# Optimization experiments

Measured on AMD Instinct MI355X. Metric: run time of the kernel, lower is better.

Reference implementation:

```python
import jax, jax.numpy as jnp
import numpy as np

N_WIRES = 9
N_QRAM_LAYERS = 3
N_QCLS_LAYERS = 5

X = jnp.array([[0, 1], [1, 0]], dtype=jnp.complex64)
CNOT = jnp.array([[1, 0, 0, 0], [0, 1, 0, 0], [0, 0, 0, 1], [0, 0, 1, 0]], dtype=jnp.complex64)


def _rx(t):
    c = jnp.cos(t / 2)
    s = jnp.sin(t / 2)
    # works for scalar t -> (2,2) or batched t [B] -> (B,2,2)
    return jnp.stack([jnp.stack([c + 0j, -1j * s], -1), jnp.stack([-1j * s, c + 0j], -1)], -2)


def _ry(t):
    c = jnp.cos(t / 2)
    s = jnp.sin(t / 2)
    return jnp.stack([jnp.stack([c, -s], -1), jnp.stack([s, c], -1)], -2).astype(jnp.complex64)


def _rz(t):
    e = jnp.exp(-0.5j * t)
    f = jnp.exp(0.5j * t)
    z = jnp.zeros_like(e)
    return jnp.stack([jnp.stack([e, z], -1), jnp.stack([z, f], -1)], -2)


def _rot(phi, theta, omega):
    # PennyLane Rot(phi, theta, omega) = RZ(omega) @ RY(theta) @ RZ(phi)
    return _rz(omega) @ _ry(theta) @ _rz(phi)


def _crz(t):
    e = jnp.exp(-0.5j * t)
    f = jnp.exp(0.5j * t)
    one = jnp.ones((), e.dtype)
    return jnp.diag(jnp.stack([one, one, e, f]))


def _crx(t):
    return jnp.eye(4, dtype=jnp.complex64).at[2:, 2:].set(_rx(t))


def apply_1q(state, U, w):
    # state: [B] + (2,)*N_WIRES ; wire w -> axis 1+w
    s = jnp.moveaxis(state, 1 + w, -1)
    if U.ndim == 3:  # per-sample gate (embedding)
        s = jnp.einsum('bij,b...j->b...i', U, s)
    else:
        s = jnp.einsum('ij,...j->...i', U, s)
    return jnp.moveaxis(s, -1, 1 + w)


def apply_2q(state, U, c, t):
    s = jnp.moveaxis(state, (1 + c, 1 + t), (-2, -1))
    shp = s.shape
    s = s.reshape(shp[:-2] + (4,))
    s = jnp.einsum('ij,...j->...i', U, s)
    return jnp.moveaxis(s.reshape(shp), (-2, -1), (1 + c, 1 + t))


def embed(state, adds):
    # AngleEmbedding: RX(adds[:, i]) on wire i
    for i in range(N_WIRES):
        state = apply_1q(state, _rx(adds[:, i]), i)
    return state


def entangle_block(state, p):
    # p: [36] = 4 params per wire-pair step
    j = 0
    for i in range(N_WIRES):
        ip = (i + 1) % N_WIRES
        state = apply_1q(state, _ry(p[j]), i)
        state = apply_1q(state, _ry(p[j + 1]), ip)
        state = apply_2q(state, CNOT, i, ip)
        state = apply_2q(state, _crz(p[j + 2]), i, ip)
        state = apply_1q(state, X, ip)
        state = apply_2q(state, _crx(p[j + 3]), i, ip)
        j += 4
    return state


def sel_layer(state, w, r):
    # one StronglyEntanglingLayers layer: Rot on each wire, then CNOT ring of range r
    for i in range(N_WIRES):
        state = apply_1q(state, _rot(w[i, 0], w[i, 1], w[i, 2]), i)
    for i in range(N_WIRES):
        state = apply_2q(state, CNOT, i, (i + r) % N_WIRES)
    return state


def circuit(adds, params, weights, params2):
    B = adds.shape[0]
    state = jnp.zeros((B,) + (2,) * N_WIRES, jnp.complex64)
    state = state.at[(slice(None),) + (0,) * N_WIRES].set(1.0)
    state = embed(state, adds)
    for l in range(N_QRAM_LAYERS):
        state = entangle_block(state, params[l * 36:(l + 1) * 36])
    for l in range(N_QRAM_LAYERS):
        r = (l % (N_WIRES - 1)) + 1  # PennyLane default ranges
        state = sel_layer(state, weights[l], r)
    for l in range(N_QCLS_LAYERS):
        state = entangle_block(state, params2[l * 36:(l + 1) * 36])
    probs = jnp.abs(state) ** 2
    p = probs.reshape(B, 2, -1).sum(-1)  # marginal over wire 0
    return p[:, 0] - p[:, 1]  # <PauliZ(0)>


def setup_inputs() -> dict:
    key = jax.random.key(0)
    k1, k2, k3, k4 = jax.random.split(key, 4)
    B = 8192
    return {
        'adds': jax.random.normal(k1, (B, N_WIRES), dtype=jnp.float32),
        'params': jax.random.normal(k2, (N_QRAM_LAYERS * 36,), dtype=jnp.float32),
        'weights': jax.random.normal(k3, (N_QRAM_LAYERS, N_WIRES, N_QRAM_LAYERS), dtype=jnp.float32),
        'params2': jax.random.normal(k4, (N_QCLS_LAYERS * 36,), dtype=jnp.float32),
    }


def reference(adds, params, weights, params2):
    return circuit(adds, params, weights, params2)
```

## Files before the change

### kernel.cpp

```cpp
#include <hip/hip_runtime.h>

#define NQ 9
#define NS 512
#define M2 1024

#define COEF_ROT_BASE (72*32)
#define COEF_R3_BASE  (COEF_ROT_BASE + 27*8)
#define COEF_FLOATS   (COEF_R3_BASE + 3*128)

typedef __attribute__((ext_vector_type(8))) short bf16x8;
typedef __attribute__((ext_vector_type(4))) float f32x4;

__device__ inline unsigned short f2bf(float f){
  unsigned int u = __float_as_uint(f);
  u += 0x7fffu + ((u >> 16) & 1u);
  return (unsigned short)(u >> 16);
}


template<int LM>
__device__ inline float lxor(float v){
  if constexpr (LM == 1)
    return __int_as_float(__builtin_amdgcn_mov_dpp(__float_as_int(v), 0xB1, 0xF, 0xF, true));
  else if constexpr (LM == 2)
    return __int_as_float(__builtin_amdgcn_mov_dpp(__float_as_int(v), 0x4E, 0xF, 0xF, true));
  else if constexpr (LM == 3)
    return __int_as_float(__builtin_amdgcn_mov_dpp(__float_as_int(v), 0x1B, 0xF, 0xF, true));
  else if constexpr (LM < 32)
    return __int_as_float(__builtin_amdgcn_ds_swizzle(__float_as_int(v), (LM<<10)|0x1F));
  else
    return __shfl_xor(v, LM);
}

template<int CM, int TM>
__device__ inline void step_h(float& ax, float& ay, int i, float2* buf,
                              const float* g){
  buf[i] = make_float2(ax, ay);
  __syncthreads();
  float2 tv = buf[i ^ TM];
  float2 cv = buf[i ^ CM];
  float2 bv = buf[i ^ (CM ^ TM)];
  int p = ((i & CM) ? 2 : 0) | ((i & TM) ? 1 : 0);
  float4 hx = *(const float4*)(g + p*4);
  float4 hy = *(const float4*)(g + 16 + p*4);
  float ox = ax, oy = ay;
  ax = hx.x*ox - hy.x*oy + hx.y*tv.x - hy.y*tv.y
     + hx.z*cv.x - hy.z*cv.y + hx.w*bv.x - hy.w*bv.y;
  ay = hx.x*oy + hy.x*ox + hx.y*tv.y + hy.y*tv.x
     + hx.z*cv.y + hy.z*cv.x + hx.w*bv.y + hy.w*bv.x;
}

template<int CM, int TM>
__device__ inline void step_swz(float& ax, float& ay, int lane, const float* g){
  float tx = lxor<TM>(ax),      ty = lxor<TM>(ay);
  float cx = lxor<CM>(ax),      cy = lxor<CM>(ay);
  float bx = lxor<(CM^TM)>(ax), by = lxor<(CM^TM)>(ay);
  int p = ((lane & CM) ? 2 : 0) | ((lane & TM) ? 1 : 0);
  float4 hx = *(const float4*)(g + p*4);
  float4 hy = *(const float4*)(g + 16 + p*4);
  float ox = ax, oy = ay;
  ax = hx.x*ox - hy.x*oy + hx.y*tx - hy.y*ty
     + hx.z*cx - hy.z*cy + hx.w*bx - hy.w*by;
  ay = hx.x*oy + hy.x*ox + hx.y*ty + hy.y*tx
     + hx.z*cy + hy.z*cx + hx.w*by + hy.w*bx;
}

__device__ inline void rot3_img(float& ax, float& ay, int i, float2* buf,
                                const float* M){
  buf[i] = make_float2(ax, ay);
  __syncthreads();
  int base = i & 63;
  float nx = 0.f, ny = 0.f;
  #pragma unroll
  for (int q = 0; q < 8; ++q){
    float2 v = buf[(q << 6) | base];
    float mx = M[q*2], my = M[q*2+1];
    nx += mx*v.x - my*v.y;
    ny += mx*v.y + my*v.x;
  }
  ax = nx; ay = ny;
}

template<int LM>
__device__ inline void rot_swz(float& ax, float& ay, int lane, const float* u){
  float px = lxor<LM>(ax), py = lxor<LM>(ay);
  float4 uu = *(const float4*)(u + ((lane & LM) ? 4 : 0));
  float nx = uu.x*ax - uu.y*ay + uu.z*px - uu.w*py;
  float ny = uu.x*ay + uu.y*ax + uu.z*py + uu.w*px;
  ax = nx; ay = ny;
}

__device__ inline void ring_rt(float& ax, float& ay, int i, float2* buf, int R){
  buf[i] = make_float2(ax, ay);
  __syncthreads();
  int s = i;
  for (int k = 8; k >= 0; --k){
    int bc = 8 - k;
    int it = k + R; if (it >= 9) it -= 9;
    int bt = 8 - it;
    s ^= ((s >> bc) & 1) << bt;
  }
  float2 v = buf[s];
  ax = v.x; ay = v.y;
}


template<int I = 0>
__device__ inline void ent_blk(float& ax, float& ay, int i, int lane,
                               float2* bufA, float2* bufB, const float* S){
  const float* g = S + I*32;
  if constexpr      (I == 0) step_h<0x100,0x080>(ax, ay, i, bufA, g);
  else if constexpr (I == 1) step_h<0x080,0x040>(ax, ay, i, bufB, g);
  else if constexpr (I == 2) step_h<0x040,0x020>(ax, ay, i, bufA, g);
  else if constexpr (I == 8) step_h<0x001,0x100>(ax, ay, i, bufB, g);
  else                       step_swz<(1<<(8-I)),(1<<(7-I))>(ax, ay, lane, g);
  if constexpr (I < 8) ent_blk<I+1>(ax, ay, i, lane, bufA, bufB, S);
}

template<int I = 3>
__device__ inline void sel_lane_rots(float& ax, float& ay, int lane,
                                     const float* ub){
  rot_swz<(1<<(8-I))>(ax, ay, lane, ub + I*8);
  if constexpr (I < 8) sel_lane_rots<I+1>(ax, ay, lane, ub);
}

__global__ __launch_bounds__(512) void sim_prep(const float* __restrict__ params,
                                                const float* __restrict__ weights,
                                                const float* __restrict__ params2,
                                                const float* __restrict__ adds,
                                                unsigned short* __restrict__ A2,
                                                unsigned short* __restrict__ cT,
                                                float* __restrict__ out, int B){
  int tid = threadIdx.x;

  if (blockIdx.x >= NS){
    int gid = (blockIdx.x - NS) * 512 + tid;
    int b = gid >> 6;
    int lane = gid & 63;
    if (b < B){
      const float* ab = adds + b * NQ;
      float cw[NQ], sw[NQ];
      #pragma unroll
      for (int w = 0; w < NQ; ++w)
        __sincosf(0.5f * ab[w], &sw[w], &cw[w]);
      float p6 = 1.f;
      #pragma unroll
      for (int w = 0; w < 6; ++w)
        p6 *= ((lane >> (5 - w)) & 1) ? sw[w] : cw[w];
      union { unsigned short u[8]; uint4 v; } pk;
      #pragma unroll
      for (int j = 0; j < 8; ++j){
        float p = p6 * (((j>>2)&1) ? sw[6] : cw[6])
                     * (((j>>1)&1) ? sw[7] : cw[7])
                     * (( j    &1) ? sw[8] : cw[8]);
        pk.u[j] = f2bf(p);
      }
      *(uint4*)(cT + (size_t)b * NS + lane*8) = pk.v;
    }
    if (gid < B) out[gid] = 0.f;
    return;
  }

  __shared__ float2 bufA[512];
  __shared__ float2 bufB[512];
  __shared__ float scoef[COEF_FLOATS];

  if (tid < 72){
    int blk = tid / 9, I = tid % 9;
    const float* p = (blk < 3) ? params + blk*36 : params2 + (blk-3)*36;
    float s0,c0,s1,c1,s2,c2,s3,c3;
    __sincosf(0.5f*p[4*I+0], &s0, &c0);
    __sincosf(0.5f*p[4*I+1], &s1, &c1);
    __sincosf(0.5f*p[4*I+2], &s2, &c2);
    __sincosf(0.5f*p[4*I+3], &s3, &c3);
    float m[4][4] = {
      { c0*c1, -c0*s1, -s0*c1,  s0*s1},
      { c0*s1,  c0*c1, -s0*s1, -s0*c1},
      { s0*c1, -s0*s1,  c0*c1, -c0*s1},
      { s0*s1,  s0*c1,  c0*s1,  c0*c1}};
    float gx[4][4], gy[4][4];
    #pragma unroll
    for (int q = 0; q < 4; ++q){
      gx[0][q] = m[1][q];  gy[0][q] = 0.f;
      gx[1][q] = m[0][q];  gy[1][q] = 0.f;
      gx[2][q] =  c3*c2*m[2][q] - s3*s2*m[3][q];
      gy[2][q] =  c3*s2*m[2][q] - s3*c2*m[3][q];
      gx[3][q] =  s3*s2*m[2][q] + c3*c2*m[3][q];
      gy[3][q] = -(s3*c2*m[2][q] + c3*s2*m[3][q]);
    }
    float* dst = scoef + tid*32;
    #pragma unroll
    for (int pp = 0; pp < 4; ++pp)
      #pragma unroll
      for (int d = 0; d < 4; ++d){
        dst[pp*4+d]    = gx[pp][pp^d];
        dst[16+pp*4+d] = gy[pp][pp^d];
      }
  } else if (tid < 99){
    int r = tid - 72;
    int l = r / 9, i = r % 9;
    const float* w = weights + l*27 + 3*i;
    float phi = w[0], th = w[1], om = w[2];
    float sT,cT,sA,cA,sB,cB;
    __sincosf(0.5f*th, &sT, &cT);
    __sincosf(0.5f*(phi+om), &sA, &cA);
    __sincosf(0.5f*(om-phi), &sB, &cB);
    float* dst = scoef + COEF_ROT_BASE + r*8;
    dst[0] =  cA*cT;  dst[1] = -sA*cT;
    dst[2] = -cB*sT;  dst[3] =  sB*sT;
    dst[4] =  cA*cT;  dst[5] =  sA*cT;
    dst[6] =  cB*sT;  dst[7] =  sB*sT;
  } else if (tid < 123){
    int idx = tid - 99;
    int l = idx >> 3, p = idx & 7;
    float e0x[3], e0y[3], e1x[3], e1y[3];
    #pragma unroll
    for (int w = 0; w < 3; ++w){
      const float* wp = weights + l*27 + 3*w;
      float phi = wp[0], th = wp[1], om = wp[2];
      float sT,cT,sA,cA,sB,cB;
      __sincosf(0.5f*th, &sT, &cT);
      __sincosf(0.5f*(phi+om), &sA, &cA);
      __sincosf(0.5f*(om-phi), &sB, &cB);
      int pw = (p >> (2 - w)) & 1;
      if (pw == 0){ e0x[w] =  cA*cT; e0y[w] = -sA*cT; e1x[w] = -cB*sT; e1y[w] =  sB*sT; }
      else        { e0x[w] =  cB*sT; e0y[w] =  sB*sT; e1x[w] =  cA*cT; e1y[w] =  sA*cT; }
    }
    float* dst = scoef + COEF_R3_BASE + l*128 + p*16;
    #pragma unroll
    for (int q = 0; q < 8; ++q){
      float rx = 1.f, ry = 0.f;
      #pragma unroll
      for (int w = 0; w < 3; ++w){
        int qw = (q >> (2 - w)) & 1;
        float fx = qw ? e1x[w] : e0x[w];
        float fy = qw ? e1y[w] : e0y[w];
        float nx = rx*fx - ry*fy;
        float ny = rx*fy + ry*fx;
        rx = nx; ry = ny;
      }
      dst[q*2]   = rx;
      dst[q*2+1] = ry;
    }
  }
  __syncthreads();

  int t = blockIdx.x;
  int i = tid;
  int lane = tid & 63;
  float ax, ay;
  int pc = __popc((unsigned)t) & 3;
  float prx = (pc==0) ? 1.f : (pc==2 ? -1.f : 0.f);
  float pry = (pc==3) ? 1.f : (pc==1 ? -1.f : 0.f);
  ax = (i == t) ? prx : 0.f;
  ay = (i == t) ? pry : 0.f;

  #pragma unroll 1
  for (int blk = 0; blk < 3; ++blk)
    ent_blk<0>(ax, ay, i, lane, bufA, bufB, scoef + blk*288);
  #pragma unroll 1
  for (int L = 0; L < 3; ++L){
    rot3_img(ax, ay, i, bufA, scoef + COEF_R3_BASE + L*128 + (i>>6)*16);
    sel_lane_rots<3>(ax, ay, lane, scoef + COEF_ROT_BASE + L*72);
    ring_rt(ax, ay, i, bufB, L + 1);
  }
  #pragma unroll 1
  for (int blk = 3; blk < 8; ++blk)
    ent_blk<0>(ax, ay, i, lane, bufA, bufB, scoef + blk*288);

  A2[(size_t)i * NS + t]        = f2bf(ax);
  A2[(size_t)(i + NS) * NS + t] = f2bf(ay);
}

__global__ __launch_bounds__(256) void gemm_out(const unsigned short* __restrict__ A2,
                                                const unsigned short* __restrict__ cT,
                                                float* __restrict__ out){
  int bx = blockIdx.x;
  int by = blockIdx.y;
  int tid = threadIdx.x;
  int wave = tid >> 6, lane = tid & 63;
  int wy = wave >> 1, wx = wave & 1;
  int lane15 = lane & 15, quad = lane >> 4;
  int rowBase = by*128 + wy*64;
  int colBase = bx*128 + wx*64;
  const short* Ap = (const short*)A2;
  const short* Bp = (const short*)cT;

  f32x4 acc[4][4];
  #pragma unroll
  for (int i = 0; i < 4; ++i)
    #pragma unroll
    for (int j = 0; j < 4; ++j)
      acc[i][j] = (f32x4){0.f, 0.f, 0.f, 0.f};

  #pragma unroll 2
  for (int k0 = 0; k0 < NS; k0 += 32){
    bf16x8 a[4], b[4];
    #pragma unroll
    for (int mi = 0; mi < 4; ++mi)
      a[mi] = *(const bf16x8*)(Ap + (size_t)(rowBase + mi*16 + lane15)*NS + k0 + quad*8);
    #pragma unroll
    for (int ni = 0; ni < 4; ++ni)
      b[ni] = *(const bf16x8*)(Bp + (size_t)(colBase + ni*16 + lane15)*NS + k0 + quad*8);
    #pragma unroll
    for (int mi = 0; mi < 4; ++mi)
      #pragma unroll
      for (int ni = 0; ni < 4; ++ni)
        acc[mi][ni] = __builtin_amdgcn_mfma_f32_16x16x32_bf16(a[mi], b[ni], acc[mi][ni], 0, 0, 0);
  }

  float sign = (by & 2) ? -1.f : 1.f;
  #pragma unroll
  for (int ni = 0; ni < 4; ++ni){
    float cs = 0.f;
    #pragma unroll
    for (int mi = 0; mi < 4; ++mi)
      #pragma unroll
      for (int r = 0; r < 4; ++r)
        cs += acc[mi][ni][r] * acc[mi][ni][r];
    cs += __shfl_xor(cs, 16);
    cs += __shfl_xor(cs, 32);
    if (quad == 0)
      atomicAdd(out + colBase + ni*16 + lane15, sign * cs);
  }
}

extern "C" void kernel_launch(void* const* d_in, const int* in_sizes, int n_in,
                              void* d_out, int out_size, void* d_ws, size_t ws_size,
                              hipStream_t stream) {
  const float* adds    = (const float*)d_in[0];
  const float* params  = (const float*)d_in[1];
  const float* weights = (const float*)d_in[2];
  const float* params2 = (const float*)d_in[3];
  float* out = (float*)d_out;
  int B = in_sizes[0] / NQ;

  unsigned short* A2 = (unsigned short*)d_ws;
  unsigned short* cT = A2 + (size_t)M2 * NS;

  int prepBlocks = (B * 64 + 511) / 512;
  hipLaunchKernelGGL(sim_prep, dim3(NS + prepBlocks), dim3(512), 0, stream,
                     params, weights, params2, adds, A2, cT, out, B);
  hipLaunchKernelGGL(gemm_out, dim3(B / 128, 8), dim3(256), 0, stream, A2, cT, out);
}
```

Measured before the change: 118.2 us.

## Merge cross-wave entangler steps into dense 16x16 and 8x8 shared-memory matrices

Each entangler block previously did four separate shared-memory exchange steps, each with a barrier. The three leading two-qubit steps (wires 0-3) are now premultiplied into one 16x16 complex matrix, and the last two steps (wires 7,8,0) into one 8x8 matrix. Each block then needs two barriered shared-memory passes instead of four, at the cost of more FLOPs per element and extra setup to build the matrices. The A2 matrix is also stored in a k-chunked layout so the GEMM loads contiguous bf16x8 vectors, and the GEMM unroll is raised.

```diff
diff --git a/kernel.cpp b/kernel.cpp
--- a/kernel.cpp
+++ b/kernel.cpp
@@ -3,10 +3,14 @@
 #define NQ 9
 #define NS 512
 #define M2 1024
-
-#define COEF_ROT_BASE (72*32)
-#define COEF_R3_BASE  (COEF_ROT_BASE + 27*8)
-#define COEF_FLOATS   (COEF_R3_BASE + 3*128)
+#define NSIMB 512
+
+#define ENT_H_BASE 0
+#define ROT_BASE   1024
+#define ROT3_BASE  1240
+#define M0123_BASE 1624
+#define M78_BASE   5720
+#define COEF_FLOATS 6744
 
 typedef __attribute__((ext_vector_type(8))) short bf16x8;
 typedef __attribute__((ext_vector_type(4))) float f32x4;
@@ -30,24 +34,6 @@
     return __int_as_float(__builtin_amdgcn_ds_swizzle(__float_as_int(v), (LM<<10)|0x1F));
   else
     return __shfl_xor(v, LM);
-}
-
-template<int CM, int TM>
-__device__ inline void step_h(float& ax, float& ay, int i, float2* buf,
-                              const float* g){
-  buf[i] = make_float2(ax, ay);
-  __syncthreads();
-  float2 tv = buf[i ^ TM];
-  float2 cv = buf[i ^ CM];
-  float2 bv = buf[i ^ (CM ^ TM)];
-  int p = ((i & CM) ? 2 : 0) | ((i & TM) ? 1 : 0);
-  float4 hx = *(const float4*)(g + p*4);
-  float4 hy = *(const float4*)(g + 16 + p*4);
-  float ox = ax, oy = ay;
-  ax = hx.x*ox - hy.x*oy + hx.y*tv.x - hy.y*tv.y
-     + hx.z*cv.x - hy.z*cv.y + hx.w*bv.x - hy.w*bv.y;
-  ay = hx.x*oy + hy.x*ox + hx.y*tv.y + hy.y*tv.x
-     + hx.z*cv.y + hy.z*cv.x + hx.w*bv.y + hy.w*bv.x;
 }
 
 template<int CM, int TM>
@@ -65,20 +51,62 @@
      + hx.z*cy + hy.z*cx + hx.w*by + hy.w*bx;
 }
 
-__device__ inline void rot3_img(float& ax, float& ay, int i, float2* buf,
-                                const float* M){
-  buf[i] = make_float2(ax, ay);
-  __syncthreads();
+__device__ inline void mrg16(float& ax, float& ay, int i, float2* xb, const float* Mt){
+  xb[i] = make_float2(ax, ay);
+  __syncthreads();
+  int p = (i >> 5) & 15;
+  const float* Mr = Mt + p*32;
+  int base = i & 31;
+  float s0x=0.f,s0y=0.f,s1x=0.f,s1y=0.f;
+  #pragma unroll
+  for (int q = 0; q < 16; q += 2){
+    float2 v0 = xb[(q<<5)|base];
+    float2 v1 = xb[((q+1)<<5)|base];
+    float m0x = Mr[q*2],   m0y = Mr[q*2+1];
+    float m1x = Mr[q*2+2], m1y = Mr[q*2+3];
+    s0x += m0x*v0.x - m0y*v0.y;  s0y += m0x*v0.y + m0y*v0.x;
+    s1x += m1x*v1.x - m1y*v1.y;  s1y += m1x*v1.y + m1y*v1.x;
+  }
+  ax = s0x + s1x; ay = s0y + s1y;
+}
+
+__device__ inline void mrg8_78(float& ax, float& ay, int i, float2* xb, const float* Mt){
+  xb[i] = make_float2(ax, ay);
+  __syncthreads();
+  int p = (((i>>1)&1)<<2) | ((i&1)<<1) | ((i>>8)&1);
+  const float* Mr = Mt + p*16;
+  int ib = i & 0x0FC;
+  float s0x=0.f,s0y=0.f,s1x=0.f,s1y=0.f;
+  #pragma unroll
+  for (int q = 0; q < 8; q += 2){
+    int j0 = ib | ((q>>2)<<1) | ((q>>1)&1);
+    float2 v0 = xb[j0];
+    float2 v1 = xb[j0 | 0x100];
+    float m0x = Mr[q*2],   m0y = Mr[q*2+1];
+    float m1x = Mr[q*2+2], m1y = Mr[q*2+3];
+    s0x += m0x*v0.x - m0y*v0.y;  s0y += m0x*v0.y + m0y*v0.x;
+    s1x += m1x*v1.x - m1y*v1.y;  s1y += m1x*v1.y + m1y*v1.x;
+  }
+  ax = s0x + s1x; ay = s0y + s1y;
+}
+
+__device__ inline void rot3R(float& ax, float& ay, int i, float2* xb, const float* Mt){
+  xb[i] = make_float2(ax, ay);
+  __syncthreads();
+  int p = i >> 6;
+  const float* Mr = Mt + p*16;
   int base = i & 63;
-  float nx = 0.f, ny = 0.f;
+  float s0x=0.f,s0y=0.f,s1x=0.f,s1y=0.f;
   #pragma unroll
-  for (int q = 0; q < 8; ++q){
-    float2 v = buf[(q << 6) | base];
-    float mx = M[q*2], my = M[q*2+1];
-    nx += mx*v.x - my*v.y;
-    ny += mx*v.y + my*v.x;
-  }
-  ax = nx; ay = ny;
+  for (int q = 0; q < 8; q += 2){
+    float2 v0 = xb[(q<<6)|base];
+    float2 v1 = xb[((q+1)<<6)|base];
+    float m0x = Mr[q*2],   m0y = Mr[q*2+1];
+    float m1x = Mr[q*2+2], m1y = Mr[q*2+3];
+    s0x += m0x*v0.x - m0y*v0.y;  s0y += m0x*v0.y + m0y*v0.x;
+    s1x += m1x*v1.x - m1y*v1.y;  s1y += m1x*v1.y + m1y*v1.x;
+  }
+  ax = s0x + s1x; ay = s0y + s1y;
 }
 
 template<int LM>
@@ -90,6 +118,12 @@
   ax = nx; ay = ny;
 }
 
+template<int I = 3>
+__device__ inline void sel_lane_rots(float& ax, float& ay, int lane, const float* ub){
+  rot_swz<(1<<(8-I))>(ax, ay, lane, ub + I*8);
+  if constexpr (I < 8) sel_lane_rots<I+1>(ax, ay, lane, ub);
+}
+
 __device__ inline void ring_rt(float& ax, float& ay, int i, float2* buf, int R){
   buf[i] = make_float2(ax, ay);
   __syncthreads();
@@ -104,25 +138,16 @@
   ax = v.x; ay = v.y;
 }
 
-
-template<int I = 0>
-__device__ inline void ent_blk(float& ax, float& ay, int i, int lane,
-                               float2* bufA, float2* bufB, const float* S){
-  const float* g = S + I*32;
-  if constexpr      (I == 0) step_h<0x100,0x080>(ax, ay, i, bufA, g);
-  else if constexpr (I == 1) step_h<0x080,0x040>(ax, ay, i, bufB, g);
-  else if constexpr (I == 2) step_h<0x040,0x020>(ax, ay, i, bufA, g);
-  else if constexpr (I == 8) step_h<0x001,0x100>(ax, ay, i, bufB, g);
-  else                       step_swz<(1<<(8-I)),(1<<(7-I))>(ax, ay, lane, g);
-  if constexpr (I < 8) ent_blk<I+1>(ax, ay, i, lane, bufA, bufB, S);
-}
-
-template<int I = 3>
-__device__ inline void sel_lane_rots(float& ax, float& ay, int lane,
-                                     const float* ub){
-  rot_swz<(1<<(8-I))>(ax, ay, lane, ub + I*8);
-  if constexpr (I < 8) sel_lane_rots<I+1>(ax, ay, lane, ub);
-}
+__device__ inline void entM(float& ax, float& ay, int i, int lane,
+                            float2* bA, float2* bB, const float* scoef, int blk){
+  mrg16(ax, ay, i, bA, scoef + M0123_BASE + blk*512);
+  step_swz<32,16>(ax, ay, lane, scoef + ENT_H_BASE + (blk*4+0)*32);
+  step_swz<16, 8>(ax, ay, lane, scoef + ENT_H_BASE + (blk*4+1)*32);
+  step_swz< 8, 4>(ax, ay, lane, scoef + ENT_H_BASE + (blk*4+2)*32);
+  step_swz< 4, 2>(ax, ay, lane, scoef + ENT_H_BASE + (blk*4+3)*32);
+  mrg8_78(ax, ay, i, bB, scoef + M78_BASE + blk*128);
+}
+
 
 __global__ __launch_bounds__(512) void sim_prep(const float* __restrict__ params,
                                                 const float* __restrict__ weights,
@@ -133,8 +158,8 @@
                                                 float* __restrict__ out, int B){
   int tid = threadIdx.x;
 
-  if (blockIdx.x >= NS){
-    int gid = (blockIdx.x - NS) * 512 + tid;
+  if (blockIdx.x >= NSIMB){
+    int gid = (blockIdx.x - NSIMB) * 512 + tid;
     int b = gid >> 6;
     int lane = gid & 63;
     if (b < B){
@@ -161,9 +186,11 @@
     return;
   }
 
-  __shared__ float2 bufA[512];
-  __shared__ float2 bufB[512];
+  __shared__ float2 ebuf[1024];
   __shared__ float scoef[COEF_FLOATS];
+  float2* ebufA = ebuf;
+  float2* ebufB = ebuf + 512;
+  float* graw = (float*)ebuf;
 
   if (tid < 72){
     int blk = tid / 9, I = tid % 9;
@@ -188,14 +215,26 @@
       gx[3][q] =  s3*s2*m[2][q] + c3*c2*m[3][q];
       gy[3][q] = -(s3*c2*m[2][q] + c3*s2*m[3][q]);
     }
-    float* dst = scoef + tid*32;
-    #pragma unroll
-    for (int pp = 0; pp < 4; ++pp)
-      #pragma unroll
-      for (int d = 0; d < 4; ++d){
-        dst[pp*4+d]    = gx[pp][pp^d];
-        dst[16+pp*4+d] = gy[pp][pp^d];
-      }
+    if (I >= 3 && I <= 6){
+      float* dst = scoef + ENT_H_BASE + (blk*4 + (I-3))*32;
+      #pragma unroll
+      for (int pp = 0; pp < 4; ++pp)
+        #pragma unroll
+        for (int d = 0; d < 4; ++d){
+          dst[pp*4+d]    = gx[pp][pp^d];
+          dst[16+pp*4+d] = gy[pp][pp^d];
+        }
+    } else {
+      float* dst = (I < 3) ? graw + (blk*3 + I)*32
+                           : graw + 768 + (blk*2 + (I-7))*32;
+      #pragma unroll
+      for (int pp = 0; pp < 4; ++pp)
+        #pragma unroll
+        for (int q = 0; q < 4; ++q){
+          dst[(pp*4+q)*2]   = gx[pp][q];
+          dst[(pp*4+q)*2+1] = gy[pp][q];
+        }
+    }
   } else if (tid < 99){
     int r = tid - 72;
     int l = r / 9, i = r % 9;
@@ -205,7 +244,7 @@
     __sincosf(0.5f*th, &sT, &cT);
     __sincosf(0.5f*(phi+om), &sA, &cA);
     __sincosf(0.5f*(om-phi), &sB, &cB);
-    float* dst = scoef + COEF_ROT_BASE + r*8;
+    float* dst = scoef + ROT_BASE + r*8;
     dst[0] =  cA*cT;  dst[1] = -sA*cT;
     dst[2] = -cB*sT;  dst[3] =  sB*sT;
     dst[4] =  cA*cT;  dst[5] =  sA*cT;
@@ -226,7 +265,7 @@
       if (pw == 0){ e0x[w] =  cA*cT; e0y[w] = -sA*cT; e1x[w] = -cB*sT; e1y[w] =  sB*sT; }
       else        { e0x[w] =  cB*sT; e0y[w] =  sB*sT; e1x[w] =  cA*cT; e1y[w] =  sA*cT; }
     }
-    float* dst = scoef + COEF_R3_BASE + l*128 + p*16;
+    float* dst = scoef + ROT3_BASE + l*128 + p*16;
     #pragma unroll
     for (int q = 0; q < 8; ++q){
       float rx = 1.f, ry = 0.f;
@@ -245,31 +284,80 @@
   }
   __syncthreads();
 
-  int t = blockIdx.x;
-  int i = tid;
-  int lane = tid & 63;
+  {
+    int blk = tid >> 6;
+    const float* G0 = graw + (blk*3+0)*32;
+    const float* G1 = graw + (blk*3+1)*32;
+    const float* G2 = graw + (blk*3+2)*32;
+    int e4 = (tid & 63) * 4;
+    #pragma unroll
+    for (int k = 0; k < 4; ++k){
+      int e = e4 + k;
+      int p = e >> 4, q = e & 15;
+      int a=(p>>3)&1, b=(p>>2)&1, c=(p>>1)&1, d=p&1;
+      int ee=(q>>3)&1, f=(q>>2)&1, g=(q>>1)&1, h=q&1;
+      float sx = 0.f, sy = 0.f;
+      #pragma unroll
+      for (int m = 0; m < 2; ++m)
+        #pragma unroll
+        for (int n = 0; n < 2; ++n){
+          const float* z2 = G2 + ((c*2+d)*4 + (n*2+h))*2;
+          const float* z1 = G1 + ((b*2+n)*4 + (m*2+g))*2;
+          const float* z0 = G0 + ((a*2+m)*4 + (ee*2+f))*2;
+          float ux = z2[0]*z1[0] - z2[1]*z1[1];
+          float uy = z2[0]*z1[1] + z2[1]*z1[0];
+          float vx = ux*z0[0] - uy*z0[1];
+          float vy = ux*z0[1] + uy*z0[0];
+          sx += vx; sy += vy;
+        }
+      scoef[M0123_BASE + blk*512 + (p*16+q)*2]   = sx;
+      scoef[M0123_BASE + blk*512 + (p*16+q)*2+1] = sy;
+    }
+    const float* G7 = graw + 768 + (blk*2+0)*32;
+    const float* G8 = graw + 768 + (blk*2+1)*32;
+    int e = tid & 63;
+    int p = e >> 3, q = e & 7;
+    int a=(p>>2)&1, b=(p>>1)&1, c=p&1;
+    int d=(q>>2)&1, ei=(q>>1)&1, f=q&1;
+    float sx = 0.f, sy = 0.f;
+    #pragma unroll
+    for (int m = 0; m < 2; ++m){
+      const float* z8 = G8 + ((b*2+c)*4 + (m*2+f))*2;
+      const float* z7 = G7 + ((a*2+m)*4 + (d*2+ei))*2;
+      sx += z8[0]*z7[0] - z8[1]*z7[1];
+      sy += z8[0]*z7[1] + z8[1]*z7[0];
+    }
+    scoef[M78_BASE + blk*128 + (p*8+q)*2]   = sx;
+    scoef[M78_BASE + blk*128 + (p*8+q)*2+1] = sy;
+  }
+  __syncthreads();
+
+  int i = tid, lane = tid & 63;
+  int col = blockIdx.x;
   float ax, ay;
-  int pc = __popc((unsigned)t) & 3;
+  int pc = __popc((unsigned)col) & 3;
   float prx = (pc==0) ? 1.f : (pc==2 ? -1.f : 0.f);
   float pry = (pc==3) ? 1.f : (pc==1 ? -1.f : 0.f);
-  ax = (i == t) ? prx : 0.f;
-  ay = (i == t) ? pry : 0.f;
+  ax = (i == col) ? prx : 0.f;
+  ay = (i == col) ? pry : 0.f;
 
   #pragma unroll 1
   for (int blk = 0; blk < 3; ++blk)
-    ent_blk<0>(ax, ay, i, lane, bufA, bufB, scoef + blk*288);
+    entM(ax, ay, i, lane, ebufA, ebufB, scoef, blk);
   #pragma unroll 1
   for (int L = 0; L < 3; ++L){
-    rot3_img(ax, ay, i, bufA, scoef + COEF_R3_BASE + L*128 + (i>>6)*16);
-    sel_lane_rots<3>(ax, ay, lane, scoef + COEF_ROT_BASE + L*72);
-    ring_rt(ax, ay, i, bufB, L + 1);
+    rot3R(ax, ay, i, ebufA, scoef + ROT3_BASE + L*128);
+    sel_lane_rots<3>(ax, ay, lane, scoef + ROT_BASE + L*72);
+    ring_rt(ax, ay, i, ebufB, L + 1);
   }
   #pragma unroll 1
   for (int blk = 3; blk < 8; ++blk)
-    ent_blk<0>(ax, ay, i, lane, bufA, bufB, scoef + blk*288);
-
-  A2[(size_t)i * NS + t]        = f2bf(ax);
-  A2[(size_t)(i + NS) * NS + t] = f2bf(ay);
+    entM(ax, ay, i, lane, ebufA, ebufB, scoef, blk);
+
+  int c = col >> 3, sub = col & 7;
+  size_t base = (size_t)c * 1024;
+  A2[(base + i)*8 + sub]       = f2bf(ax);
+  A2[(base + 512 + i)*8 + sub] = f2bf(ay);
 }
 
 __global__ __launch_bounds__(256) void gemm_out(const unsigned short* __restrict__ A2,
@@ -283,7 +371,7 @@
   int lane15 = lane & 15, quad = lane >> 4;
   int rowBase = by*128 + wy*64;
   int colBase = bx*128 + wx*64;
-  const short* Ap = (const short*)A2;
+  const bf16x8* Ap8 = (const bf16x8*)A2;
   const short* Bp = (const short*)cT;
 
   f32x4 acc[4][4];
@@ -293,12 +381,13 @@
     for (int j = 0; j < 4; ++j)
       acc[i][j] = (f32x4){0.f, 0.f, 0.f, 0.f};
 
-  #pragma unroll 2
+  #pragma unroll 4
   for (int k0 = 0; k0 < NS; k0 += 32){
     bf16x8 a[4], b[4];
+    int c = (k0 >> 3) + quad;
     #pragma unroll
     for (int mi = 0; mi < 4; ++mi)
-      a[mi] = *(const bf16x8*)(Ap + (size_t)(rowBase + mi*16 + lane15)*NS + k0 + quad*8);
+      a[mi] = Ap8[(size_t)c*1024 + rowBase + mi*16 + lane15];
     #pragma unroll
     for (int ni = 0; ni < 4; ++ni)
       b[ni] = *(const bf16x8*)(Bp + (size_t)(colBase + ni*16 + lane15)*NS + k0 + quad*8);
@@ -339,7 +428,7 @@
   unsigned short* cT = A2 + (size_t)M2 * NS;
 
   int prepBlocks = (B * 64 + 511) / 512;
-  hipLaunchKernelGGL(sim_prep, dim3(NS + prepBlocks), dim3(512), 0, stream,
+  hipLaunchKernelGGL(sim_prep, dim3(NSIMB + prepBlocks), dim3(512), 0, stream,
                      params, weights, params2, adds, A2, cT, out, B);
   hipLaunchKernelGGL(gemm_out, dim3(B / 128, 8), dim3(256), 0, stream, A2, cT, out);
 }
```

Measured after the change: 113.8 us. 3.8% less time.
